# Performance work log

Measured on AMD Instinct MI355X. Metric: run time of the kernel, lower is better.

Reference implementation:

```python
import jax, jax.numpy as jnp
import numpy as np

B, S, D, K = 16, 1024, 512, 4
DIL = (1, 2, 4, 8)
EPS_BN = 1e-5
EPS_LN = 1e-5


def _edge_conv1d(x, w, b, dilation):
    # x: [B, C, S], w: [O, C, k]; replicate ('edge') padding keeps length S
    p = (w.shape[-1] - 1) * dilation // 2
    xp = jnp.pad(x, ((0, 0), (0, 0), (p, p)), mode='edge')
    y = jax.lax.conv_general_dilated(xp, w, (1,), 'VALID', rhs_dilation=(dilation,),
                                     dimension_numbers=('NCH', 'OIH', 'NCH'))
    return y + b[None, :, None]


def setup_inputs() -> dict:
    key = jax.random.key(0)
    ks = jax.random.split(key, 16)
    g = lambda i, shape, s: jax.random.normal(ks[i], shape, jnp.float32) * s
    return {
        'x': g(0, (B, S, D), 1.0),
        'conv_w': g(1, (4, D, D, 3), 0.02),
        'conv_b': jnp.zeros((4, D), jnp.float32),
        'fusion_w': g(2, (D, 4 * D), 0.02),
        'fusion_b': jnp.zeros((D,), jnp.float32),
        'refine_w': g(3, (D, D, 3), 0.02),
        'refine_b': jnp.zeros((D,), jnp.float32),
        'hyp1_w': g(4, (D, D, 3), 0.02),
        'hyp1_b': jnp.zeros((D,), jnp.float32),
        'bn_gamma': jnp.ones((D,), jnp.float32),
        'bn_beta': jnp.zeros((D,), jnp.float32),
        'hyp2_w': g(5, (D // 2, D, 3), 0.02),
        'hyp2_b': jnp.zeros((D // 2,), jnp.float32),
        'proj_w': g(6, (2 * K, D // 2), 0.05),
        'proj_b': jnp.zeros((2 * K,), jnp.float32),
        'gate_w': g(7, (D, D), 0.02),
        'gate_b': jnp.zeros((D,), jnp.float32),
        'base_w': g(8, (D, D), 0.02),
        'base_b': jnp.zeros((D,), jnp.float32),
        'wav_w': g(9, (K, D, D), 0.02),
        'wav_b': jnp.zeros((K, D), jnp.float32),
        'ln_gamma': jnp.ones((D,), jnp.float32),
        'ln_beta': jnp.zeros((D,), jnp.float32),
    }


def _forward(x, conv_w, conv_b, fusion_w, fusion_b, refine_w, refine_b,
             hyp1_w, hyp1_b, bn_gamma, bn_beta, hyp2_w, hyp2_b,
             proj_w, proj_b, gate_w, gate_b, base_w, base_b,
             wav_w, wav_b, ln_gamma, ln_beta):
    residual = x
    x_in = jnp.transpose(x, (0, 2, 1))                      # [B, D, S]
    # ---- FFT trend/seasonal split ----
    fx = jnp.fft.rfft(x_in, axis=2)
    cutoff = S // 10
    mask = (jnp.arange(fx.shape[2]) < cutoff).astype(fx.dtype)
    x_seasonal = jnp.fft.irfft(fx * mask, n=S, axis=2)       # [B, D, S]
    x_smooth = x_seasonal
    x_spike = x_in - x_seasonal
    # ---- iterative dilated-conv smoothing (dropout = identity, eval mode) ----
    for _ in range(2):  # iterations
        outs = [jax.nn.gelu(_edge_conv1d(x_smooth, conv_w[i], conv_b[i], DIL[i]),
                            approximate=False)
                for i in range(4)]
        x_concat = jnp.concatenate(outs, axis=1)             # [B, 4D, S]
        x_smooth = jnp.einsum('oc,bcs->bos', fusion_w, x_concat) + fusion_b[None, :, None]
        x_spike = _edge_conv1d(x_in - x_smooth, refine_w, refine_b, 1)
    x_smooth_t = jnp.transpose(x_smooth, (0, 2, 1))          # [B, S, D]
    x_spike_t = jnp.transpose(x_spike, (0, 2, 1))            # [B, S, D]
    # ---- hypernet (BatchNorm in eval mode: running mean 0, var 1) ----
    h = _edge_conv1d(x_smooth, hyp1_w, hyp1_b, 1)
    h = h / jnp.sqrt(1.0 + EPS_BN) * bn_gamma[None, :, None] + bn_beta[None, :, None]
    h = jax.nn.silu(h)
    h = jax.nn.silu(_edge_conv1d(h, hyp2_w, hyp2_b, 1))      # [B, D/2, S]
    cnn_feat = jnp.mean(h, axis=2)                           # AdaptiveAvgPool1d(1)
    params = (cnn_feat @ proj_w.T + proj_b).reshape(B, 1, K, 2)
    dyn_a = jax.nn.softplus(params[..., 0]) + 0.01           # [B, 1, K]
    dyn_b = jax.nn.sigmoid(params[..., 1]) * S               # [B, 1, K]
    # ---- wavelet-KAN base path: Linear(silu(x_smooth)) ----
    base_out = jnp.einsum('bsd,ed->bse', jax.nn.silu(x_smooth_t), base_w) + base_b
    # ---- wavelet path: mexican-hat wavelets over sequence positions ----
    pos = jnp.arange(S, dtype=x.dtype)[None, :, None]        # [1, S, 1]
    u = (pos - dyn_b) / dyn_a                                # [B, S, K]
    c = 2.0 / (np.sqrt(3.0) * np.pi ** 0.25)
    psi = c * (1.0 - u * u) * jnp.exp(-0.5 * u * u)          # [B, S, K]
    z = jnp.einsum('bsd,kde->bkse', x_spike_t, wav_w)        # per-wavelet linear
    kan_out = jnp.einsum('bsk,bkse->bse', psi, z) + jnp.einsum('bsk,ke->bse', psi, wav_b)
    amp = jax.nn.sigmoid(base_out @ gate_w.T + gate_b) * 2.0
    x_out = base_out + kan_out * amp
    # ---- residual + LayerNorm ----
    y = x_out + residual
    mu = jnp.mean(y, axis=-1, keepdims=True)
    var = jnp.var(y, axis=-1, keepdims=True)
    return (y - mu) / jnp.sqrt(var + EPS_LN) * ln_gamma + ln_beta


def reference(x, conv_w, conv_b, fusion_w, fusion_b, refine_w, refine_b,
              hyp1_w, hyp1_b, bn_gamma, bn_beta, hyp2_w, hyp2_b,
              proj_w, proj_b, gate_w, gate_b, base_w, base_b,
              wav_w, wav_b, ln_gamma, ln_beta):
    return _forward(x, conv_w, conv_b, fusion_w, fusion_b, refine_w, refine_b,
                    hyp1_w, hyp1_b, bn_gamma, bn_beta, hyp2_w, hyp2_b,
                    proj_w, proj_b, gate_w, gate_b, base_w, base_b,
                    wav_w, wav_b, ln_gamma, ln_beta)
```

## Files before the change

kernel.cpp:

```cpp
#include <hip/hip_runtime.h>
#include <hip/hip_bf16.h>
#include <math.h>

#define NB 16
#define SS 1024
#define DD 512
#define SP 1040
#define HD 256

typedef unsigned short US;
typedef short bf16x8 __attribute__((ext_vector_type(8)));
typedef float f32x4 __attribute__((ext_vector_type(4)));
typedef __attribute__((address_space(1))) const void gv1;
typedef __attribute__((address_space(3))) void lv3;

static __device__ __forceinline__ float b2sf(US u){ return __uint_as_float(((unsigned)u)<<16); }
static __device__ __forceinline__ US f2b(float f){
  __hip_bfloat16 h = __float2bfloat16(f);
  union { __hip_bfloat16 h; US u; } c; c.h = h; return c.u;
}
static __device__ __forceinline__ float rd(const void* __restrict__ p, long i, int isf){
  return isf ? ((const float*)p)[i] : b2sf(((const US*)p)[i]);
}

__global__ void k_detect(const void* __restrict__ x, int* __restrict__ flag){
  const US* u = (const US*)x;
  int t = threadIdx.x;
  float m = 0.f;
  for (int i = t; i < 4096; i += 256){
    float v = fabsf(b2sf(u[i]));
    if (isnan(v) || isinf(v)) v = 1e30f;
    m = fmaxf(m, v);
  }
  for (int off = 32; off; off >>= 1) m = fmaxf(m, __shfl_down(m, off));
  __shared__ float sh[4];
  if ((t & 63) == 0) sh[t >> 6] = m;
  __syncthreads();
  if (t == 0){
    float mm = fmaxf(fmaxf(sh[0], sh[1]), fmaxf(sh[2], sh[3]));
    flag[0] = (mm > 1e6f) ? 1 : 0;
  }
}

__global__ void k_cvt_f(const void* __restrict__ s, float* __restrict__ d, long n, const int* __restrict__ fl){
  int isf = fl[0];
  long i = (long)blockIdx.x*256 + threadIdx.x;
  if (i < n) d[i] = rd(s, i, isf);
}
__global__ void k_cvt_b(const void* __restrict__ s, US* __restrict__ d, long n, const int* __restrict__ fl){
  int isf = fl[0];
  long i = (long)blockIdx.x*256 + threadIdx.x;
  if (i < n) d[i] = f2b(rd(s, i, isf));
}
__global__ void k_repack3(const void* __restrict__ src, US* __restrict__ dst, int O, int C, const int* __restrict__ fl){
  int isf = fl[0];
  long i = (long)blockIdx.x*256 + threadIdx.x;
  long n = (long)O*3*C;
  if (i >= n) return;
  int o = (int)(i / (3*C)); int r = (int)(i - (long)o*3*C); int t = r / C; int c = r - t*C;
  dst[i] = f2b(rd(src, ((long)o*C + c)*3 + t, isf));
}
__global__ void k_repack_wav(const void* __restrict__ src, US* __restrict__ dst, const int* __restrict__ fl){
  int isf = fl[0];
  long i = (long)blockIdx.x*256 + threadIdx.x;
  if (i >= 4L*DD*DD) return;
  int k = (int)(i >> 18); long r = i & ((1<<18)-1); int e = (int)(r >> 9); int d = (int)(r & 511);
  dst[i] = f2b(rd(src, ((long)(k*DD + d))*DD + e, isf));
}
__global__ void k_build_g(float* __restrict__ g){
  int d = blockIdx.x*256 + threadIdx.x;
  if (d >= SS) return;
  float s = 1.f;
  for (int k = 1; k < 102; ++k){
    int r = (k*d) & (SS-1);
    s += 2.f * cosf(6.28318530718f * (float)r * (1.f/SS));
  }
  g[d] = s * (1.f/SS);
}
__global__ void k_build_cmat(const float* __restrict__ g, US* __restrict__ cm){
  int i = blockIdx.x*256 + threadIdx.x;
  if (i >= SS*SS) return;
  int t = i >> 10, s = i & (SS-1);
  cm[i] = f2b(g[(s - t) & (SS-1)]);
}
__global__ __launch_bounds__(256) void k_transpose_b(const void* __restrict__ x, US* __restrict__ xt, const int* __restrict__ fl){
  int isf = fl[0];
  __shared__ float tl[32][33];
  int b = blockIdx.z, s0 = blockIdx.x*32, d0 = blockIdx.y*32;
  int tx = threadIdx.x & 31, ty = threadIdx.x >> 5;
  for (int i = ty; i < 32; i += 8)
    tl[i][tx] = rd(x, ((long)(b*SS + s0+i))*DD + d0+tx, isf);
  __syncthreads();
  for (int i = ty; i < 32; i += 8)
    xt[((long)(b*DD + d0+i))*SS + s0+tx] = f2b(tl[tx][i]);
}
__global__ void k_pad_b(const US* __restrict__ src, const void* __restrict__ xsub, US* __restrict__ dst, const int* __restrict__ fl){
  long i = (long)blockIdx.x*256 + threadIdx.x;
  const long TOT = (long)NB*SP*128;
  if (i >= TOT) return;
  int c4 = (int)(i & 127);
  int j  = (int)((i >> 7) % SP);
  int b  = (int)(i / (128L*SP));
  int sr = j - 8; sr = sr < 0 ? 0 : (sr > SS-1 ? SS-1 : sr);
  long si = ((long)(b*SS + sr))*DD + c4*4;
  ushort4 sv = *(const ushort4*)&src[si];
  float v0=b2sf(sv.x), v1=b2sf(sv.y), v2=b2sf(sv.z), v3=b2sf(sv.w);
  if (xsub){
    if (fl[0]){
      float4 xv = *(const float4*)((const float*)xsub + si);
      v0 = xv.x - v0; v1 = xv.y - v1; v2 = xv.z - v2; v3 = xv.w - v3;
    } else {
      ushort4 xv = *(const ushort4*)((const US*)xsub + si);
      v0 = b2sf(xv.x) - v0; v1 = b2sf(xv.y) - v1; v2 = b2sf(xv.z) - v2; v3 = b2sf(xv.w) - v3;
    }
  }
  ushort4 o; o.x=f2b(v0); o.y=f2b(v1); o.z=f2b(v2); o.w=f2b(v3);
  *(ushort4*)&dst[((long)(b*SP + j))*DD + c4*4] = o;
}
__global__ void k_silu_b(const US* __restrict__ s, US* __restrict__ d){
  long i = (long)blockIdx.x*256 + threadIdx.x;
  if (i >= (long)NB*SS*DD/4) return;
  ushort4 sv = *(const ushort4*)&s[i*4];
  float v[4] = {b2sf(sv.x), b2sf(sv.y), b2sf(sv.z), b2sf(sv.w)};
  ushort4 o;
  US* op = (US*)&o;
  #pragma unroll
  for (int r = 0; r < 4; r++){ float t = v[r]; op[r] = f2b(t/(1.f + expf(-t))); }
  *(ushort4*)&d[i*4] = o;
}

template<int EPI, bool TAPPED>
__global__ __launch_bounds__(256) void k_mfma(
    const US* __restrict__ A, const US* __restrict__ Bact, void* __restrict__ Out,
    int NYB, int K, long sBbytes, int ldbB, int dil,
    long sOut, int ldo, int moff,
    const float* __restrict__ bias, const float* __restrict__ s1v, const float* __restrict__ s2v,
    const float* __restrict__ psiP)
{
  __shared__ alignas(16) US shb[2*128*64];
  __shared__ float psh[(EPI==4) ? 512 : 4];
  US* As = shb;
  US* Bs = shb + 128*64;
  const int bx = blockIdx.x;
  const int ny = bx % NYB;
  const int b  = bx / NYB;
  const int m0 = blockIdx.y*128, n0 = ny*128;
  const int dd = (TAPPED && dil < 0) ? (1 << (m0 >> 9)) : dil;
  const char* Bb = (const char*)Bact + (long)b*sBbytes;
  const int tid = threadIdx.x;
  const int lane = tid & 63, w = tid >> 6;
  const int wr = w >> 1, wc = w & 1;
  const int col = lane & 15, g = lane >> 4;

  if (EPI == 4){
    for (int i = tid; i < 512; i += 256)
      psh[i] = psiP[(long)b*4096 + (i >> 7)*SS + n0 + (i & 127)];
  }

  f32x4 acc[4][4];
  f32x4 facc[4][4];
  if (EPI == 4){
    #pragma unroll
    for (int i = 0; i < 4; i++)
      #pragma unroll
      for (int j = 0; j < 4; j++) facc[i][j] = (f32x4){0.f,0.f,0.f,0.f};
  }

  int rows_[4], sls_[4];
  #pragma unroll
  for (int i = 0; i < 4; i++){
    int c = w*256 + i*64 + lane;
    rows_[i] = c >> 3;
    sls_[i] = (c & 7) ^ ((c >> 3) & 7);
  }

  const int NKC = (EPI == 4) ? 4 : 1;
  for (int kc = 0; kc < NKC; ++kc){
    #pragma unroll
    for (int i = 0; i < 4; i++)
      #pragma unroll
      for (int j = 0; j < 4; j++) acc[i][j] = (f32x4){0.f,0.f,0.f,0.f};

    for (int k0 = 0; k0 < K; k0 += 64){
      const int c0 = TAPPED ? (k0 & 511) : k0;
      const int srowOff = TAPPED ? (8 + ((k0 >> 9) - 1)*dd) : 0;
      __syncthreads();
      #pragma unroll
      for (int i = 0; i < 4; i++){
        const long arow = (long)(m0 + rows_[i]) + (EPI==4 ? kc*512 : 0);
        const char* ga = (const char*)A + (arow*K + k0)*2 + sls_[i]*16;
        __builtin_amdgcn_global_load_lds((gv1*)ga, (lv3*)&As[(w*256 + i*64)*8], 16, 0, 0);
        const char* gb = Bb + (long)(n0 + rows_[i] + srowOff)*ldbB + c0*2 + sls_[i]*16;
        __builtin_amdgcn_global_load_lds((gv1*)gb, (lv3*)&Bs[(w*256 + i*64)*8], 16, 0, 0);
      }
      __syncthreads();
      #pragma unroll
      for (int kk = 0; kk < 2; kk++){
        bf16x8 af[4], bf[4];
        #pragma unroll
        for (int f = 0; f < 4; f++){
          int rowa = wr*64 + f*16 + col;
          int sla = (g + kk*4) ^ (rowa & 7);
          af[f] = *(const bf16x8*)&As[rowa*64 + sla*8];
          int rowb = wc*64 + f*16 + col;
          int slb = (g + kk*4) ^ (rowb & 7);
          bf[f] = *(const bf16x8*)&Bs[rowb*64 + slb*8];
        }
        #pragma unroll
        for (int fm = 0; fm < 4; fm++)
          #pragma unroll
          for (int fn = 0; fn < 4; fn++)
            acc[fm][fn] = __builtin_amdgcn_mfma_f32_16x16x32_bf16(af[fm], bf[fn], acc[fm][fn], 0, 0, 0);
      }
    }

    if (EPI == 4){
      #pragma unroll
      for (int fm = 0; fm < 4; fm++){
        const int mm_l = wr*64 + fm*16 + g*4;
        float bb[4];
        #pragma unroll
        for (int r = 0; r < 4; r++) bb[r] = bias[kc*512 + m0 + mm_l + r];
        #pragma unroll
        for (int fn = 0; fn < 4; fn++){
          float p = psh[kc*128 + wc*64 + fn*16 + col];
          #pragma unroll
          for (int r = 0; r < 4; r++)
            facc[fm][fn][r] += p * (acc[fm][fn][r] + bb[r]);
        }
      }
    }
  }

  __syncthreads();
  US* tile = shb;
  #pragma unroll
  for (int fm = 0; fm < 4; fm++){
    const int mm_l = wr*64 + fm*16 + g*4;
    float bb[4];
    if (EPI <= 3){
      #pragma unroll
      for (int r = 0; r < 4; r++) bb[r] = bias[m0 + mm_l + r];
    }
    #pragma unroll
    for (int fn = 0; fn < 4; fn++){
      const int nn_l = wc*64 + fn*16 + col;
      f32x4 v = (EPI == 4) ? facc[fm][fn] : acc[fm][fn];
      if (EPI == 5){
        #pragma unroll
        for (int r = 0; r < 4; r++){
          int row = mm_l + r;
          int byte = row*256 + ((nn_l*2) ^ ((row & 7) << 4));
          *(US*)((char*)tile + byte) = f2b(v[r]);
        }
      } else {
        US pk[4];
        #pragma unroll
        for (int r = 0; r < 4; r++){
          float val = v[r];
          if (EPI <= 3) val += bb[r];
          if (EPI == 1) val = 0.5f*val*(1.f + erff(val*0.70710678f));
          if (EPI == 2){ int m = m0 + mm_l + r; val = val*(s1v[m]*0.99999500f) + s2v[m]; val = val/(1.f + expf(-val)); }
          if (EPI == 3){ val = val/(1.f + expf(-val)); }
          pk[r] = f2b(val);
        }
        int byte = nn_l*256 + ((mm_l*2) ^ ((nn_l & 7) << 4));
        *(int2*)((char*)tile + byte) = *(int2*)pk;
      }
    }
  }
  __syncthreads();
  const int r0 = tid >> 4, c = tid & 15;
  #pragma unroll
  for (int p = 0; p < 8; p++){
    int r = p*16 + r0;
    int4 vv = *(const int4*)((const char*)tile + r*256 + ((c*16) ^ ((r & 7) << 4)));
    long obase = (EPI == 5) ? ((long)b*sOut + (long)(m0 + r)*ldo + n0)
                            : ((long)b*sOut + (long)(n0 + r)*ldo + moff + m0);
    *(int4*)((US*)Out + obase + c*8) = vv;
  }
}

__global__ __launch_bounds__(256) void k_pool(const US* __restrict__ h2, float* __restrict__ feat){
  int b = blockIdx.x, c = threadIdx.x;
  float s = 0.f;
  for (int t = 0; t < SS; t++) s += b2sf(h2[((long)(b*SS + t))*HD + c]);
  feat[b*HD + c] = s * (1.f/SS);
}
__global__ void k_params(const float* __restrict__ feat, const float* __restrict__ pw,
                         const float* __restrict__ pb, float* __restrict__ dynA, float* __restrict__ dynB){
  int t = threadIdx.x;
  if (t >= 128) return;
  int b = t >> 3, j = t & 7;
  float s = pb[j];
  for (int c = 0; c < HD; c++) s += feat[b*HD + c]*pw[j*HD + c];
  int k = j >> 1;
  if ((j & 1) == 0){
    float sp = s > 20.f ? s : log1pf(expf(s));
    dynA[b*4 + k] = sp + 0.01f;
  } else {
    dynB[b*4 + k] = 1024.f/(1.f + expf(-s));
  }
}
__global__ void k_psi(const float* __restrict__ dynA, const float* __restrict__ dynB, float* __restrict__ psi){
  int i = blockIdx.x*256 + threadIdx.x;
  if (i >= NB*4*SS) return;
  int b = i >> 12, k = (i >> 10) & 3, s = i & (SS-1);
  float u = ((float)s - dynB[b*4 + k]) / dynA[b*4 + k];
  psi[i] = 0.86732507f*(1.f - u*u)*expf(-0.5f*u*u);
}
__global__ __launch_bounds__(128) void k_final(const US* __restrict__ base, const US* __restrict__ kan,
    const US* __restrict__ gate, const void* __restrict__ x,
    void* __restrict__ out, const float* __restrict__ lng, const float* __restrict__ lnb,
    const int* __restrict__ fl){
  int isf = fl[0];
  long row = blockIdx.x;
  int t = threadIdx.x;
  long off = row*DD + t*4;
  ushort4 bs = *(const ushort4*)&base[off];
  ushort4 gt = *(const ushort4*)&gate[off];
  ushort4 kn = *(const ushort4*)&kan[off];
  float xv[4];
  if (isf){ float4 q = *(const float4*)((const float*)x + off); xv[0]=q.x; xv[1]=q.y; xv[2]=q.z; xv[3]=q.w; }
  else { ushort4 q = *(const ushort4*)((const US*)x + off); xv[0]=b2sf(q.x); xv[1]=b2sf(q.y); xv[2]=b2sf(q.z); xv[3]=b2sf(q.w); }
  float bv[4] = {b2sf(bs.x), b2sf(bs.y), b2sf(bs.z), b2sf(bs.w)};
  float gv[4] = {b2sf(gt.x), b2sf(gt.y), b2sf(gt.z), b2sf(gt.w)};
  const US* kp = (const US*)&kn;
  float y[4];
  float sm = 0.f, ssq = 0.f;
  #pragma unroll
  for (int r = 0; r < 4; r++){
    float amp = 2.f/(1.f + expf(-gv[r]));
    y[r] = bv[r] + b2sf(kp[r])*amp + xv[r];
    sm += y[r]; ssq += y[r]*y[r];
  }
  for (int o = 32; o; o >>= 1){ sm += __shfl_down(sm, o); ssq += __shfl_down(ssq, o); }
  __shared__ float sh[4];
  int lane = t & 63, wid = t >> 6;
  if (lane == 0){ sh[wid*2] = sm; sh[wid*2+1] = ssq; }
  __syncthreads();
  float S1 = sh[0] + sh[2], S2 = sh[1] + sh[3];
  float mean = S1*(1.f/DD), var = S2*(1.f/DD) - mean*mean;
  float rstd = rsqrtf(var + 1e-5f);
  #pragma unroll
  for (int r = 0; r < 4; r++){
    int d = t*4 + r;
    float val = (y[r] - mean)*rstd*lng[d] + lnb[d];
    if (isf) ((float*)out)[off + r] = val;
    else     ((US*)out)[off + r] = f2b(val);
  }
}

extern "C" void kernel_launch(void* const* d_in, const int* in_sizes, int n_in,
                              void* d_out, int out_size, void* d_ws, size_t ws_size,
                              hipStream_t stream){
  const void* x       = d_in[0];
  const void* conv_w  = d_in[1];
  const void* conv_b  = d_in[2];
  const void* fusion_w= d_in[3];
  const void* fusion_b= d_in[4];
  const void* refine_w= d_in[5];
  const void* refine_b= d_in[6];
  const void* hyp1_w  = d_in[7];
  const void* hyp1_b  = d_in[8];
  const void* bn_g    = d_in[9];
  const void* bn_b    = d_in[10];
  const void* hyp2_w  = d_in[11];
  const void* hyp2_b  = d_in[12];
  const void* proj_w  = d_in[13];
  const void* proj_b  = d_in[14];
  const void* gate_w  = d_in[15];
  const void* gate_b  = d_in[16];
  const void* base_w  = d_in[17];
  const void* base_b  = d_in[18];
  const void* wav_w   = d_in[19];
  const void* wav_b   = d_in[20];
  const void* ln_g    = d_in[21];
  const void* ln_b    = d_in[22];

  char* wsb = (char*)d_ws;
  long off = 0;
  auto AA = [&](long bytes)->char*{ char* p = wsb + off; off += (bytes + 255) & ~255L; return p; };
  US* padG  = (US*)AA((long)NB*SP*DD*2);
  US* smA   = (US*)AA((long)NB*SS*DD*2);
  US* smB   = (US*)AA((long)NB*SS*DD*2);
  US* xTh   = (US*)AA((long)NB*SS*DD*2);
  US* cc    = (US*)AA((long)NB*SS*2048*2);
  US* baseB = (US*)AA((long)NB*SS*DD*2);
  US* Wc  = (US*)AA(4L*512*1536*2);
  US* Wr  = (US*)AA(512L*1536*2);
  US* Wh1 = (US*)AA(512L*1536*2);
  US* Wh2 = (US*)AA(256L*1536*2);
  US* Wwv = (US*)AA(4L*512*512*2);
  US* Fw  = (US*)AA(512L*2048*2);
  US* BW  = (US*)AA(512L*512*2);
  US* GW  = (US*)AA(512L*512*2);
  US* Cm  = (US*)AA(1024L*1024*2);
  float* gvec = (float*)AA(1024*4);
  float* cb_f = (float*)AA(2048*4);
  float* fz_b = (float*)AA(512*4);
  float* rf_b = (float*)AA(512*4);
  float* h1_b = (float*)AA(512*4);
  float* h2_b = (float*)AA(256*4);
  float* bs_b = (float*)AA(512*4);
  float* gt_b = (float*)AA(512*4);
  float* wv_b = (float*)AA(2048*4);
  float* bngf = (float*)AA(512*4);
  float* bnbf = (float*)AA(512*4);
  float* pwf  = (float*)AA(2048*4);
  float* pbf  = (float*)AA(8*4);
  float* lngf = (float*)AA(512*4);
  float* lnbf = (float*)AA(512*4);
  float* feat = (float*)AA(16*256*4);
  float* dynA = (float*)AA(64*4);
  float* dynB = (float*)AA(64*4);
  float* psi  = (float*)AA((long)NB*4*SS*4);
  int* flag   = (int*)AA(64);
  if ((size_t)off > ws_size) return;
  US* h2    = cc;
  US* siluS = cc + 16777216;
  US* kanb  = cc;

  auto g1 = [](long n){ return dim3((unsigned)((n + 255)/256)); };
  const long sAct = (long)SS*DD*2;
  const long sPad = (long)SP*DD*2;
  const long sCC  = (long)SS*2048*2;
  const long oAct = (long)SS*DD;
  const long oCC  = (long)SS*2048;
  const long oH2  = (long)SS*HD;

  k_detect<<<1, 256, 0, stream>>>(x, flag);

  k_repack3<<<g1(2048L*512*3), 256, 0, stream>>>(conv_w, Wc, 2048, 512, flag);
  k_repack3<<<g1(512L*512*3), 256, 0, stream>>>(refine_w, Wr, 512, 512, flag);
  k_repack3<<<g1(512L*512*3), 256, 0, stream>>>(hyp1_w, Wh1, 512, 512, flag);
  k_repack3<<<g1(256L*512*3), 256, 0, stream>>>(hyp2_w, Wh2, 256, 512, flag);
  k_repack_wav<<<g1(4L*512*512), 256, 0, stream>>>(wav_w, Wwv, flag);
  k_cvt_b<<<g1(512L*2048), 256, 0, stream>>>(fusion_w, Fw, 512L*2048, flag);
  k_cvt_b<<<g1(512L*512), 256, 0, stream>>>(base_w, BW, 512L*512, flag);
  k_cvt_b<<<g1(512L*512), 256, 0, stream>>>(gate_w, GW, 512L*512, flag);
  k_cvt_f<<<g1(2048), 256, 0, stream>>>(conv_b, cb_f, 2048, flag);
  k_cvt_f<<<g1(512), 256, 0, stream>>>(fusion_b, fz_b, 512, flag);
  k_cvt_f<<<g1(512), 256, 0, stream>>>(refine_b, rf_b, 512, flag);
  k_cvt_f<<<g1(512), 256, 0, stream>>>(hyp1_b, h1_b, 512, flag);
  k_cvt_f<<<g1(256), 256, 0, stream>>>(hyp2_b, h2_b, 256, flag);
  k_cvt_f<<<g1(512), 256, 0, stream>>>(base_b, bs_b, 512, flag);
  k_cvt_f<<<g1(512), 256, 0, stream>>>(gate_b, gt_b, 512, flag);
  k_cvt_f<<<g1(2048), 256, 0, stream>>>(wav_b, wv_b, 2048, flag);
  k_cvt_f<<<g1(512), 256, 0, stream>>>(bn_g, bngf, 512, flag);
  k_cvt_f<<<g1(512), 256, 0, stream>>>(bn_b, bnbf, 512, flag);
  k_cvt_f<<<g1(2048), 256, 0, stream>>>(proj_w, pwf, 2048, flag);
  k_cvt_f<<<g1(8), 256, 0, stream>>>(proj_b, pbf, 8, flag);
  k_cvt_f<<<g1(512), 256, 0, stream>>>(ln_g, lngf, 512, flag);
  k_cvt_f<<<g1(512), 256, 0, stream>>>(ln_b, lnbf, 512, flag);
  k_build_g<<<g1(SS), 256, 0, stream>>>(gvec);
  k_build_cmat<<<g1((long)SS*SS), 256, 0, stream>>>(gvec, Cm);
  k_transpose_b<<<dim3(SS/32, DD/32, NB), 256, 0, stream>>>(x, xTh, flag);

  k_mfma<5,false><<<dim3(4*NB, 8), 256, 0, stream>>>(Cm, xTh, smA,
      4, 1024, (long)DD*SS*2, SS*2, 0, oAct, DD, 0, nullptr, nullptr, nullptr, nullptr);

  US* cur = smA; US* nxt = smB;
  for (int it = 0; it < 2; ++it){
    k_pad_b<<<g1((long)NB*SP*128), 256, 0, stream>>>(cur, nullptr, padG, flag);
    k_mfma<1,true><<<dim3(8*NB, 16), 256, 0, stream>>>(Wc, padG, cc,
        8, 1536, sPad, DD*2, -1, oCC, 2048, 0, cb_f, nullptr, nullptr, nullptr);
    k_mfma<0,false><<<dim3(8*NB, 4), 256, 0, stream>>>(Fw, cc, nxt,
        8, 2048, sCC, 4096, 0, oAct, DD, 0, fz_b, nullptr, nullptr, nullptr);
    US* t = cur; cur = nxt; nxt = t;
  }

  k_pad_b<<<g1((long)NB*SP*128), 256, 0, stream>>>(cur, x, padG, flag);
  k_mfma<0,true><<<dim3(8*NB, 4), 256, 0, stream>>>(Wr, padG, smB,
      8, 1536, sPad, DD*2, 1, oAct, DD, 0, rf_b, nullptr, nullptr, nullptr);

  k_pad_b<<<g1((long)NB*SP*128), 256, 0, stream>>>(cur, nullptr, padG, flag);
  k_mfma<2,true><<<dim3(8*NB, 4), 256, 0, stream>>>(Wh1, padG, xTh,
      8, 1536, sPad, DD*2, 1, oAct, DD, 0, h1_b, bngf, bnbf, nullptr);
  k_pad_b<<<g1((long)NB*SP*128), 256, 0, stream>>>(xTh, nullptr, padG, flag);
  k_mfma<3,true><<<dim3(8*NB, 2), 256, 0, stream>>>(Wh2, padG, h2,
      8, 1536, sPad, DD*2, 1, oH2, HD, 0, h2_b, nullptr, nullptr, nullptr);
  k_pool<<<NB, 256, 0, stream>>>(h2, feat);
  k_params<<<1, 128, 0, stream>>>(feat, pwf, pbf, dynA, dynB);
  k_psi<<<g1(NB*4*SS), 256, 0, stream>>>(dynA, dynB, psi);

  k_silu_b<<<g1((long)NB*SS*DD/4), 256, 0, stream>>>(cur, siluS);
  k_mfma<0,false><<<dim3(8*NB, 4), 256, 0, stream>>>(BW, siluS, baseB,
      8, 512, sAct, DD*2, 0, oAct, DD, 0, bs_b, nullptr, nullptr, nullptr);
  k_mfma<0,false><<<dim3(8*NB, 4), 256, 0, stream>>>(GW, baseB, padG,
      8, 512, sAct, DD*2, 0, oAct, DD, 0, gt_b, nullptr, nullptr, nullptr);

  k_mfma<4,false><<<dim3(8*NB, 4), 256, 0, stream>>>(Wwv, smB, kanb,
      8, 512, sAct, DD*2, 0, oAct, DD, 0, wv_b, nullptr, nullptr, psi);

  k_final<<<NB*SS, 128, 0, stream>>>(baseB, kanb, padG, x, d_out, lngf, lnbf, flag);
}
```

Measured before the change: 767.2 us.

## Drop padded activation copies by clamping tap rows inside GEMM loads

The separate edge-padding kernels that copied activations into a padded buffer before each tapped conv GEMM are removed. The GEMM now clamps the shifted source row to [0, S-1] when it loads B tiles, which gives replicate padding directly. The x-minus-seasonal difference and the SiLU are fused into one elementwise pass, and the many weight and bias conversion launches are merged into two table-driven kernels. Pooling is split into two stages for more parallelism. The clamp adds a little index arithmetic to the GEMM's inner load loop and changes the buffer aliasing.

```diff
diff --git a/kernel.cpp b/kernel.cpp
--- a/kernel.cpp
+++ b/kernel.cpp
@@ -5,7 +5,6 @@
 #define NB 16
 #define SS 1024
 #define DD 512
-#define SP 1040
 #define HD 256
 
 typedef unsigned short US;
@@ -42,31 +41,36 @@
   }
 }
 
-__global__ void k_cvt_f(const void* __restrict__ s, float* __restrict__ d, long n, const int* __restrict__ fl){
+struct WTab { const void* src[8]; long start[9]; int type[8]; int C[8]; };
+__global__ void k_prep_w(WTab wt, US* __restrict__ dst, const int* __restrict__ fl){
   int isf = fl[0];
   long i = (long)blockIdx.x*256 + threadIdx.x;
-  if (i < n) d[i] = rd(s, i, isf);
-}
-__global__ void k_cvt_b(const void* __restrict__ s, US* __restrict__ d, long n, const int* __restrict__ fl){
+  if (i >= wt.start[8]) return;
+  int s = 0;
+  while (i >= wt.start[s+1]) s++;
+  long r = i - wt.start[s];
+  long si;
+  if (wt.type[s] == 0){
+    int C = wt.C[s]; long oc3 = 3L*C;
+    int o = (int)(r / oc3); int rr = (int)(r - (long)o*oc3); int t = rr / C; int c = rr - t*C;
+    si = ((long)o*C + c)*3 + t;
+  } else if (wt.type[s] == 1){
+    int k = (int)(r >> 18); int e = (int)((r >> 9) & 511); int d = (int)(r & 511);
+    si = ((long)(k*512 + d))*512 + e;
+  } else si = r;
+  dst[i] = f2b(rd(wt.src[s], si, isf));
+}
+
+struct FTab { const void* src[14]; int start[15]; };
+__global__ void k_cvt_all(FTab ft, float* __restrict__ dst, const int* __restrict__ fl){
   int isf = fl[0];
-  long i = (long)blockIdx.x*256 + threadIdx.x;
-  if (i < n) d[i] = f2b(rd(s, i, isf));
-}
-__global__ void k_repack3(const void* __restrict__ src, US* __restrict__ dst, int O, int C, const int* __restrict__ fl){
-  int isf = fl[0];
-  long i = (long)blockIdx.x*256 + threadIdx.x;
-  long n = (long)O*3*C;
-  if (i >= n) return;
-  int o = (int)(i / (3*C)); int r = (int)(i - (long)o*3*C); int t = r / C; int c = r - t*C;
-  dst[i] = f2b(rd(src, ((long)o*C + c)*3 + t, isf));
-}
-__global__ void k_repack_wav(const void* __restrict__ src, US* __restrict__ dst, const int* __restrict__ fl){
-  int isf = fl[0];
-  long i = (long)blockIdx.x*256 + threadIdx.x;
-  if (i >= 4L*DD*DD) return;
-  int k = (int)(i >> 18); long r = i & ((1<<18)-1); int e = (int)(r >> 9); int d = (int)(r & 511);
-  dst[i] = f2b(rd(src, ((long)(k*DD + d))*DD + e, isf));
-}
+  int i = blockIdx.x*256 + threadIdx.x;
+  if (i >= ft.start[14]) return;
+  int s = 0;
+  while (i >= ft.start[s+1]) s++;
+  dst[i] = rd(ft.src[s], i - ft.start[s], isf);
+}
+
 __global__ void k_build_g(float* __restrict__ g){
   int d = blockIdx.x*256 + threadIdx.x;
   if (d >= SS) return;
@@ -94,46 +98,32 @@
   for (int i = ty; i < 32; i += 8)
     xt[((long)(b*DD + d0+i))*SS + s0+tx] = f2b(tl[tx][i]);
 }
-__global__ void k_pad_b(const US* __restrict__ src, const void* __restrict__ xsub, US* __restrict__ dst, const int* __restrict__ fl){
-  long i = (long)blockIdx.x*256 + threadIdx.x;
-  const long TOT = (long)NB*SP*128;
-  if (i >= TOT) return;
-  int c4 = (int)(i & 127);
-  int j  = (int)((i >> 7) % SP);
-  int b  = (int)(i / (128L*SP));
-  int sr = j - 8; sr = sr < 0 ? 0 : (sr > SS-1 ? SS-1 : sr);
-  long si = ((long)(b*SS + sr))*DD + c4*4;
-  ushort4 sv = *(const ushort4*)&src[si];
-  float v0=b2sf(sv.x), v1=b2sf(sv.y), v2=b2sf(sv.z), v3=b2sf(sv.w);
-  if (xsub){
-    if (fl[0]){
-      float4 xv = *(const float4*)((const float*)xsub + si);
-      v0 = xv.x - v0; v1 = xv.y - v1; v2 = xv.z - v2; v3 = xv.w - v3;
-    } else {
-      ushort4 xv = *(const ushort4*)((const US*)xsub + si);
-      v0 = b2sf(xv.x) - v0; v1 = b2sf(xv.y) - v1; v2 = b2sf(xv.z) - v2; v3 = b2sf(xv.w) - v3;
-    }
-  }
-  ushort4 o; o.x=f2b(v0); o.y=f2b(v1); o.z=f2b(v2); o.w=f2b(v3);
-  *(ushort4*)&dst[((long)(b*SP + j))*DD + c4*4] = o;
-}
-__global__ void k_silu_b(const US* __restrict__ s, US* __restrict__ d){
+__global__ void k_diff_silu(const US* __restrict__ sm, const void* __restrict__ x,
+                            US* __restrict__ diff, US* __restrict__ sils, const int* __restrict__ fl){
+  int isf = fl[0];
   long i = (long)blockIdx.x*256 + threadIdx.x;
   if (i >= (long)NB*SS*DD/4) return;
-  ushort4 sv = *(const ushort4*)&s[i*4];
-  float v[4] = {b2sf(sv.x), b2sf(sv.y), b2sf(sv.z), b2sf(sv.w)};
-  ushort4 o;
-  US* op = (US*)&o;
-  #pragma unroll
-  for (int r = 0; r < 4; r++){ float t = v[r]; op[r] = f2b(t/(1.f + expf(-t))); }
-  *(ushort4*)&d[i*4] = o;
+  ushort4 s4 = *(const ushort4*)&sm[i*4];
+  float sv[4] = {b2sf(s4.x), b2sf(s4.y), b2sf(s4.z), b2sf(s4.w)};
+  float xv[4];
+  if (isf){ float4 q = *(const float4*)((const float*)x + i*4); xv[0]=q.x; xv[1]=q.y; xv[2]=q.z; xv[3]=q.w; }
+  else { ushort4 q = *(const ushort4*)((const US*)x + i*4); xv[0]=b2sf(q.x); xv[1]=b2sf(q.y); xv[2]=b2sf(q.z); xv[3]=b2sf(q.w); }
+  ushort4 d4, l4;
+  US* dp = (US*)&d4; US* lp = (US*)&l4;
+  #pragma unroll
+  for (int r = 0; r < 4; r++){
+    dp[r] = f2b(xv[r] - sv[r]);
+    lp[r] = f2b(sv[r]/(1.f + expf(-sv[r])));
+  }
+  *(ushort4*)&diff[i*4] = d4;
+  *(ushort4*)&sils[i*4] = l4;
 }
 
 template<int EPI, bool TAPPED>
 __global__ __launch_bounds__(256) void k_mfma(
     const US* __restrict__ A, const US* __restrict__ Bact, void* __restrict__ Out,
     int NYB, int K, long sBbytes, int ldbB, int dil,
-    long sOut, int ldo, int moff,
+    long sOut, int ldo,
     const float* __restrict__ bias, const float* __restrict__ s1v, const float* __restrict__ s2v,
     const float* __restrict__ psiP)
 {
@@ -183,14 +173,16 @@
 
     for (int k0 = 0; k0 < K; k0 += 64){
       const int c0 = TAPPED ? (k0 & 511) : k0;
-      const int srowOff = TAPPED ? (8 + ((k0 >> 9) - 1)*dd) : 0;
+      const int tapoff = TAPPED ? (((k0 >> 9) - 1)*dd) : 0;
       __syncthreads();
       #pragma unroll
       for (int i = 0; i < 4; i++){
         const long arow = (long)(m0 + rows_[i]) + (EPI==4 ? kc*512 : 0);
         const char* ga = (const char*)A + (arow*K + k0)*2 + sls_[i]*16;
         __builtin_amdgcn_global_load_lds((gv1*)ga, (lv3*)&As[(w*256 + i*64)*8], 16, 0, 0);
-        const char* gb = Bb + (long)(n0 + rows_[i] + srowOff)*ldbB + c0*2 + sls_[i]*16;
+        int brow = n0 + rows_[i] + tapoff;
+        if (TAPPED) brow = brow < 0 ? 0 : (brow > SS-1 ? SS-1 : brow);
+        const char* gb = Bb + (long)brow*ldbB + c0*2 + sls_[i]*16;
         __builtin_amdgcn_global_load_lds((gv1*)gb, (lv3*)&Bs[(w*256 + i*64)*8], 16, 0, 0);
       }
       __syncthreads();
@@ -276,15 +268,23 @@
     int r = p*16 + r0;
     int4 vv = *(const int4*)((const char*)tile + r*256 + ((c*16) ^ ((r & 7) << 4)));
     long obase = (EPI == 5) ? ((long)b*sOut + (long)(m0 + r)*ldo + n0)
-                            : ((long)b*sOut + (long)(n0 + r)*ldo + moff + m0);
+                            : ((long)b*sOut + (long)(n0 + r)*ldo + m0);
     *(int4*)((US*)Out + obase + c*8) = vv;
   }
 }
 
-__global__ __launch_bounds__(256) void k_pool(const US* __restrict__ h2, float* __restrict__ feat){
+__global__ __launch_bounds__(256) void k_pool1(const US* __restrict__ h2, float* __restrict__ part){
+  int blk = blockIdx.x;
+  int b = blk >> 3, ch = blk & 7;
+  int c = threadIdx.x;
+  float s = 0.f;
+  for (int t = ch*128; t < ch*128 + 128; t++) s += b2sf(h2[((long)(b*SS + t))*HD + c]);
+  part[(blk << 8) | c] = s;
+}
+__global__ __launch_bounds__(256) void k_pool2(const float* __restrict__ part, float* __restrict__ feat){
   int b = blockIdx.x, c = threadIdx.x;
   float s = 0.f;
-  for (int t = 0; t < SS; t++) s += b2sf(h2[((long)(b*SS + t))*HD + c]);
+  for (int ch = 0; ch < 8; ch++) s += part[((b*8 + ch) << 8) | c];
   feat[b*HD + c] = s * (1.f/SS);
 }
 __global__ void k_params(const float* __restrict__ feat, const float* __restrict__ pw,
@@ -381,49 +381,52 @@
   char* wsb = (char*)d_ws;
   long off = 0;
   auto AA = [&](long bytes)->char*{ char* p = wsb + off; off += (bytes + 255) & ~255L; return p; };
-  US* padG  = (US*)AA((long)NB*SP*DD*2);
   US* smA   = (US*)AA((long)NB*SS*DD*2);
   US* smB   = (US*)AA((long)NB*SS*DD*2);
   US* xTh   = (US*)AA((long)NB*SS*DD*2);
   US* cc    = (US*)AA((long)NB*SS*2048*2);
   US* baseB = (US*)AA((long)NB*SS*DD*2);
-  US* Wc  = (US*)AA(4L*512*1536*2);
-  US* Wr  = (US*)AA(512L*1536*2);
-  US* Wh1 = (US*)AA(512L*1536*2);
-  US* Wh2 = (US*)AA(256L*1536*2);
-  US* Wwv = (US*)AA(4L*512*512*2);
-  US* Fw  = (US*)AA(512L*2048*2);
-  US* BW  = (US*)AA(512L*512*2);
-  US* GW  = (US*)AA(512L*512*2);
-  US* Cm  = (US*)AA(1024L*1024*2);
+  US* WBLK  = (US*)AA(7733248L*2);
+  US* Cm    = (US*)AA(1024L*1024*2);
   float* gvec = (float*)AA(1024*4);
-  float* cb_f = (float*)AA(2048*4);
-  float* fz_b = (float*)AA(512*4);
-  float* rf_b = (float*)AA(512*4);
-  float* h1_b = (float*)AA(512*4);
-  float* h2_b = (float*)AA(256*4);
-  float* bs_b = (float*)AA(512*4);
-  float* gt_b = (float*)AA(512*4);
-  float* wv_b = (float*)AA(2048*4);
-  float* bngf = (float*)AA(512*4);
-  float* bnbf = (float*)AA(512*4);
-  float* pwf  = (float*)AA(2048*4);
-  float* pbf  = (float*)AA(8*4);
-  float* lngf = (float*)AA(512*4);
-  float* lnbf = (float*)AA(512*4);
+  float* FBLK = (float*)AA(11016L*4);
   float* feat = (float*)AA(16*256*4);
+  float* part = (float*)AA(16*8*256*4);
   float* dynA = (float*)AA(64*4);
   float* dynB = (float*)AA(64*4);
   float* psi  = (float*)AA((long)NB*4*SS*4);
   int* flag   = (int*)AA(64);
   if ((size_t)off > ws_size) return;
-  US* h2    = cc;
-  US* siluS = cc + 16777216;
-  US* kanb  = cc;
+
+  US* Wc  = WBLK;
+  US* Wr  = Wc  + 3145728L;
+  US* Wh1 = Wr  + 786432L;
+  US* Wh2 = Wh1 + 786432L;
+  US* Wwv = Wh2 + 393216L;
+  US* Fw  = Wwv + 1048576L;
+  US* BW  = Fw  + 1048576L;
+  US* GW  = BW  + 262144L;
+  float* cb_f = FBLK;
+  float* fz_b = cb_f + 2048;
+  float* rf_b = fz_b + 512;
+  float* h1_b = rf_b + 512;
+  float* h2_b = h1_b + 512;
+  float* bs_b = h2_b + 256;
+  float* gt_b = bs_b + 512;
+  float* wv_b = gt_b + 512;
+  float* bngf = wv_b + 2048;
+  float* bnbf = bngf + 512;
+  float* pwf  = bnbf + 512;
+  float* pbf  = pwf  + 2048;
+  float* lngf = pbf  + 8;
+  float* lnbf = lngf + 512;
+  US* diff  = cc;
+  US* h2b   = cc;
+  US* kanb  = cc + 8388608L;
+  US* siluS = cc + 16777216L;
 
   auto g1 = [](long n){ return dim3((unsigned)((n + 255)/256)); };
   const long sAct = (long)SS*DD*2;
-  const long sPad = (long)SP*DD*2;
   const long sCC  = (long)SS*2048*2;
   const long oAct = (long)SS*DD;
   const long oCC  = (long)SS*2048;
@@ -431,67 +434,64 @@
 
   k_detect<<<1, 256, 0, stream>>>(x, flag);
 
-  k_repack3<<<g1(2048L*512*3), 256, 0, stream>>>(conv_w, Wc, 2048, 512, flag);
-  k_repack3<<<g1(512L*512*3), 256, 0, stream>>>(refine_w, Wr, 512, 512, flag);
-  k_repack3<<<g1(512L*512*3), 256, 0, stream>>>(hyp1_w, Wh1, 512, 512, flag);
-  k_repack3<<<g1(256L*512*3), 256, 0, stream>>>(hyp2_w, Wh2, 256, 512, flag);
-  k_repack_wav<<<g1(4L*512*512), 256, 0, stream>>>(wav_w, Wwv, flag);
-  k_cvt_b<<<g1(512L*2048), 256, 0, stream>>>(fusion_w, Fw, 512L*2048, flag);
-  k_cvt_b<<<g1(512L*512), 256, 0, stream>>>(base_w, BW, 512L*512, flag);
-  k_cvt_b<<<g1(512L*512), 256, 0, stream>>>(gate_w, GW, 512L*512, flag);
-  k_cvt_f<<<g1(2048), 256, 0, stream>>>(conv_b, cb_f, 2048, flag);
-  k_cvt_f<<<g1(512), 256, 0, stream>>>(fusion_b, fz_b, 512, flag);
-  k_cvt_f<<<g1(512), 256, 0, stream>>>(refine_b, rf_b, 512, flag);
-  k_cvt_f<<<g1(512), 256, 0, stream>>>(hyp1_b, h1_b, 512, flag);
-  k_cvt_f<<<g1(256), 256, 0, stream>>>(hyp2_b, h2_b, 256, flag);
-  k_cvt_f<<<g1(512), 256, 0, stream>>>(base_b, bs_b, 512, flag);
-  k_cvt_f<<<g1(512), 256, 0, stream>>>(gate_b, gt_b, 512, flag);
-  k_cvt_f<<<g1(2048), 256, 0, stream>>>(wav_b, wv_b, 2048, flag);
-  k_cvt_f<<<g1(512), 256, 0, stream>>>(bn_g, bngf, 512, flag);
-  k_cvt_f<<<g1(512), 256, 0, stream>>>(bn_b, bnbf, 512, flag);
-  k_cvt_f<<<g1(2048), 256, 0, stream>>>(proj_w, pwf, 2048, flag);
-  k_cvt_f<<<g1(8), 256, 0, stream>>>(proj_b, pbf, 8, flag);
-  k_cvt_f<<<g1(512), 256, 0, stream>>>(ln_g, lngf, 512, flag);
-  k_cvt_f<<<g1(512), 256, 0, stream>>>(ln_b, lnbf, 512, flag);
+  {
+    WTab wt;
+    const void* srcs[8] = {conv_w, refine_w, hyp1_w, hyp2_w, wav_w, fusion_w, base_w, gate_w};
+    long sizes[8] = {3145728, 786432, 786432, 393216, 1048576, 1048576, 262144, 262144};
+    int types[8] = {0,0,0,0,1,2,2,2};
+    int Cs[8]    = {512,512,512,512,0,0,0,0};
+    long acc_ = 0;
+    for (int i = 0; i < 8; i++){ wt.src[i]=srcs[i]; wt.start[i]=acc_; wt.type[i]=types[i]; wt.C[i]=Cs[i]; acc_ += sizes[i]; }
+    wt.start[8] = acc_;
+    k_prep_w<<<g1(acc_), 256, 0, stream>>>(wt, WBLK, flag);
+  }
+  {
+    FTab ft;
+    const void* srcs[14] = {conv_b, fusion_b, refine_b, hyp1_b, hyp2_b, base_b, gate_b,
+                            wav_b, bn_g, bn_b, proj_w, proj_b, ln_g, ln_b};
+    int sizes[14] = {2048,512,512,512,256,512,512,2048,512,512,2048,8,512,512};
+    int acc_ = 0;
+    for (int i = 0; i < 14; i++){ ft.src[i]=srcs[i]; ft.start[i]=acc_; acc_ += sizes[i]; }
+    ft.start[14] = acc_;
+    k_cvt_all<<<g1(acc_), 256, 0, stream>>>(ft, FBLK, flag);
+  }
   k_build_g<<<g1(SS), 256, 0, stream>>>(gvec);
   k_build_cmat<<<g1((long)SS*SS), 256, 0, stream>>>(gvec, Cm);
   k_transpose_b<<<dim3(SS/32, DD/32, NB), 256, 0, stream>>>(x, xTh, flag);
 
   k_mfma<5,false><<<dim3(4*NB, 8), 256, 0, stream>>>(Cm, xTh, smA,
-      4, 1024, (long)DD*SS*2, SS*2, 0, oAct, DD, 0, nullptr, nullptr, nullptr, nullptr);
+      4, 1024, (long)DD*SS*2, SS*2, 0, oAct, DD, nullptr, nullptr, nullptr, nullptr);
 
   US* cur = smA; US* nxt = smB;
   for (int it = 0; it < 2; ++it){
-    k_pad_b<<<g1((long)NB*SP*128), 256, 0, stream>>>(cur, nullptr, padG, flag);
-    k_mfma<1,true><<<dim3(8*NB, 16), 256, 0, stream>>>(Wc, padG, cc,
-        8, 1536, sPad, DD*2, -1, oCC, 2048, 0, cb_f, nullptr, nullptr, nullptr);
+    k_mfma<1,true><<<dim3(8*NB, 16), 256, 0, stream>>>(Wc, cur, cc,
+        8, 1536, sAct, DD*2, -1, oCC, 2048, cb_f, nullptr, nullptr, nullptr);
     k_mfma<0,false><<<dim3(8*NB, 4), 256, 0, stream>>>(Fw, cc, nxt,
-        8, 2048, sCC, 4096, 0, oAct, DD, 0, fz_b, nullptr, nullptr, nullptr);
+        8, 2048, sCC, 4096, 0, oAct, DD, fz_b, nullptr, nullptr, nullptr);
     US* t = cur; cur = nxt; nxt = t;
   }
 
-  k_pad_b<<<g1((long)NB*SP*128), 256, 0, stream>>>(cur, x, padG, flag);
-  k_mfma<0,true><<<dim3(8*NB, 4), 256, 0, stream>>>(Wr, padG, smB,
-      8, 1536, sPad, DD*2, 1, oAct, DD, 0, rf_b, nullptr, nullptr, nullptr);
-
-  k_pad_b<<<g1((long)NB*SP*128), 256, 0, stream>>>(cur, nullptr, padG, flag);
-  k_mfma<2,true><<<dim3(8*NB, 4), 256, 0, stream>>>(Wh1, padG, xTh,
-      8, 1536, sPad, DD*2, 1, oAct, DD, 0, h1_b, bngf, bnbf, nullptr);
-  k_pad_b<<<g1((long)NB*SP*128), 256, 0, stream>>>(xTh, nullptr, padG, flag);
-  k_mfma<3,true><<<dim3(8*NB, 2), 256, 0, stream>>>(Wh2, padG, h2,
-      8, 1536, sPad, DD*2, 1, oH2, HD, 0, h2_b, nullptr, nullptr, nullptr);
-  k_pool<<<NB, 256, 0, stream>>>(h2, feat);
+  k_diff_silu<<<g1((long)NB*SS*DD/4), 256, 0, stream>>>(cur, x, diff, siluS, flag);
+
+  k_mfma<0,true><<<dim3(8*NB, 4), 256, 0, stream>>>(Wr, diff, smB,
+      8, 1536, sAct, DD*2, 1, oAct, DD, rf_b, nullptr, nullptr, nullptr);
+
+  k_mfma<2,true><<<dim3(8*NB, 4), 256, 0, stream>>>(Wh1, cur, xTh,
+      8, 1536, sAct, DD*2, 1, oAct, DD, h1_b, bngf, bnbf, nullptr);
+  k_mfma<3,true><<<dim3(8*NB, 2), 256, 0, stream>>>(Wh2, xTh, h2b,
+      8, 1536, sAct, DD*2, 1, oH2, HD, h2_b, nullptr, nullptr, nullptr);
+  k_pool1<<<NB*8, 256, 0, stream>>>(h2b, part);
+  k_pool2<<<NB, 256, 0, stream>>>(part, feat);
   k_params<<<1, 128, 0, stream>>>(feat, pwf, pbf, dynA, dynB);
   k_psi<<<g1(NB*4*SS), 256, 0, stream>>>(dynA, dynB, psi);
 
-  k_silu_b<<<g1((long)NB*SS*DD/4), 256, 0, stream>>>(cur, siluS);
   k_mfma<0,false><<<dim3(8*NB, 4), 256, 0, stream>>>(BW, siluS, baseB,
-      8, 512, sAct, DD*2, 0, oAct, DD, 0, bs_b, nullptr, nullptr, nullptr);
-  k_mfma<0,false><<<dim3(8*NB, 4), 256, 0, stream>>>(GW, baseB, padG,
-      8, 512, sAct, DD*2, 0, oAct, DD, 0, gt_b, nullptr, nullptr, nullptr);
+      8, 512, sAct, DD*2, 0, oAct, DD, bs_b, nullptr, nullptr, nullptr);
+  k_mfma<0,false><<<dim3(8*NB, 4), 256, 0, stream>>>(GW, baseB, xTh,
+      8, 512, sAct, DD*2, 0, oAct, DD, gt_b, nullptr, nullptr, nullptr);
 
   k_mfma<4,false><<<dim3(8*NB, 4), 256, 0, stream>>>(Wwv, smB, kanb,
-      8, 512, sAct, DD*2, 0, oAct, DD, 0, wv_b, nullptr, nullptr, psi);
-
-  k_final<<<NB*SS, 128, 0, stream>>>(baseB, kanb, padG, x, d_out, lngf, lnbf, flag);
-}
+      8, 512, sAct, DD*2, 0, oAct, DD, wv_b, nullptr, nullptr, psi);
+
+  k_final<<<NB*SS, 128, 0, stream>>>(baseB, kanb, xTh, x, d_out, lngf, lnbf, flag);
+}
```

Result: faster. 680.4 us (-11.3%).
